# Performance work log

Hardware: AMD Instinct MI355X
Metric: run time of the kernel (lower is better)

The kernel has to match this reference:

```python
import jax, jax.numpy as jnp
import numpy as np

DIM = 768
NUM_HEADS = 12
HEAD_DIM = DIM // NUM_HEADS
ALL_HEAD_DIM = HEAD_DIM * NUM_HEADS
SCALE = HEAD_DIM ** -0.5


def setup_inputs() -> dict:
    key = jax.random.key(0)
    k1, k2, k3, k4 = jax.random.split(key, 4)
    B, N = 8, 1024
    x = jax.random.normal(k1, (B, N, DIM), dtype=jnp.float32)
    # qkv_bias=False -> no qkv bias; proj has bias (nn.Linear default)
    w_qkv = jax.random.normal(k2, (DIM, 3 * ALL_HEAD_DIM), dtype=jnp.float32) * (DIM ** -0.5)
    w_proj = jax.random.normal(k3, (ALL_HEAD_DIM, DIM), dtype=jnp.float32) * (ALL_HEAD_DIM ** -0.5)
    b_proj = jax.random.normal(k4, (DIM,), dtype=jnp.float32) * 0.02
    return {"x": x, "w_qkv": w_qkv, "w_proj": w_proj, "b_proj": b_proj}


def reference(x, w_qkv, w_proj, b_proj):
    B, N, C = x.shape
    qkv = (x @ w_qkv).reshape(B, N, 3, NUM_HEADS, HEAD_DIM)
    qkv = jnp.transpose(qkv, (2, 0, 3, 1, 4))  # [3, B, H, N, D]
    q, k, v = qkv[0], qkv[1], qkv[2]
    attn = jax.nn.softmax(jnp.einsum('bhnd,bhmd->bhnm', q * SCALE, k), axis=-1)
    out = jnp.einsum('bhnm,bhmd->bhnd', attn, v)  # [B, H, N, D]
    out = jnp.transpose(out, (0, 2, 1, 3)).reshape(B, N, ALL_HEAD_DIM)
    return out @ w_proj + b_proj
```

## Files before the change

kernel.cpp:

```cpp
#include <hip/hip_runtime.h>

#define NH 12
#define HD 64
#define SEQ 1024
#define BATCH 8
#define DIM 768
#define QKVN 2304
#define ROWS 8192

typedef __bf16 bf16x8 __attribute__((ext_vector_type(8)));
typedef float f32x4 __attribute__((ext_vector_type(4)));
typedef unsigned short u16x8 __attribute__((ext_vector_type(8)));
typedef unsigned short u16x4 __attribute__((ext_vector_type(4)));
typedef short s16x4 __attribute__((ext_vector_type(4)));

__device__ __forceinline__ unsigned short f2bf(float f) {
  union { float f; unsigned int u; } c; c.f = f;
  unsigned int u = c.u;
  u += 0x7fffu + ((u >> 16) & 1u);
  return (unsigned short)(u >> 16);
}

__device__ __forceinline__ void gload_lds16(const unsigned short* g, unsigned short* l) {
  __builtin_amdgcn_global_load_lds(
      (const __attribute__((address_space(1))) void*)g,
      (__attribute__((address_space(3))) void*)l, 16, 0, 0);
}

__global__ void cvt_bf16(const float* __restrict__ src, unsigned short* __restrict__ dst, int n4) {
  int i = blockIdx.x * 256 + threadIdx.x;
  if (i >= n4) return;
  float4 v = ((const float4*)src)[i];
  u16x4 o;
  o.x = f2bf(v.x); o.y = f2bf(v.y); o.z = f2bf(v.z); o.w = f2bf(v.w);
  ((u16x4*)dst)[i] = o;
}

__global__ void transpose_bf16(const float* __restrict__ src, unsigned short* __restrict__ dst,
                               int R, int C) {
  __shared__ float tile[32][33];
  int tx = threadIdx.x & 31, ty = threadIdx.x >> 5;
  int c0 = blockIdx.x * 32, r0 = blockIdx.y * 32;
#pragma unroll
  for (int i = 0; i < 4; ++i)
    tile[ty + i * 8][tx] = src[(size_t)(r0 + ty + i * 8) * C + c0 + tx];
  __syncthreads();
#pragma unroll
  for (int i = 0; i < 4; ++i)
    dst[(size_t)(c0 + ty + i * 8) * R + r0 + tx] = f2bf(tile[tx][ty + i * 8]);
}

template <bool BF16_OUT, bool SCALE_Q>
__global__ __launch_bounds__(256, 3) void gemm128(
    const unsigned short* __restrict__ A, const unsigned short* __restrict__ BT,
    void* __restrict__ Cout, const float* __restrict__ bias, int M, int N, int K) {
  __shared__ unsigned short As[128 * 32];
  __shared__ unsigned short Bs[128 * 32];
  const int tid = threadIdx.x;
  const int wave = tid >> 6, lane = tid & 63, quad = lane >> 4, l16 = lane & 15;
  const int wm = wave >> 1, wn = wave & 1;
  const int bm = blockIdx.y * 128, bn = blockIdx.x * 128;

  f32x4 zero4 = {0.f, 0.f, 0.f, 0.f};
  f32x4 acc[4][4];
#pragma unroll
  for (int i = 0; i < 4; ++i)
#pragma unroll
    for (int j = 0; j < 4; ++j) acc[i][j] = zero4;

  const int nkt = K >> 5;
  for (int kt = 0; kt < nkt; ++kt) {
    __syncthreads();
    const int k0 = kt * 32;
#pragma unroll
    for (int i = 0; i < 2; ++i) {
      int c0 = wave * 64 + 256 * i;
      int c = c0 + lane;
      int r = c >> 2, kc = c & 3;
      gload_lds16(A + (size_t)(bm + r) * K + k0 + kc * 8, &As[c0 * 8]);
    }
#pragma unroll
    for (int i = 0; i < 2; ++i) {
      int c0 = wave * 64 + 256 * i;
      int c = c0 + lane;
      int r = c >> 2, kc = c & 3;
      gload_lds16(BT + (size_t)(bn + r) * K + k0 + kc * 8, &Bs[c0 * 8]);
    }
    __syncthreads();
    bf16x8 af[4], bf[4];
#pragma unroll
    for (int mt = 0; mt < 4; ++mt)
      af[mt] = *(const bf16x8*)&As[(wm * 64 + mt * 16 + l16) * 32 + quad * 8];
#pragma unroll
    for (int nt = 0; nt < 4; ++nt)
      bf[nt] = *(const bf16x8*)&Bs[(wn * 64 + nt * 16 + l16) * 32 + quad * 8];
#pragma unroll
    for (int mt = 0; mt < 4; ++mt)
#pragma unroll
      for (int nt = 0; nt < 4; ++nt)
        acc[mt][nt] = __builtin_amdgcn_mfma_f32_16x16x32_bf16(af[mt], bf[nt], acc[mt][nt], 0, 0, 0);
  }
#pragma unroll
  for (int mt = 0; mt < 4; ++mt)
#pragma unroll
    for (int nt = 0; nt < 4; ++nt) {
      int col = bn + wn * 64 + nt * 16 + l16;
      float bv = BF16_OUT ? 0.f : bias[col];
      float scl = (SCALE_Q && col < DIM) ? 0.125f : 1.0f;
#pragma unroll
      for (int r = 0; r < 4; ++r) {
        int row = bm + wm * 64 + mt * 16 + quad * 4 + r;
        float v = acc[mt][nt][r];
        if (BF16_OUT)
          ((unsigned short*)Cout)[(size_t)row * N + col] = f2bf(v * scl);
        else
          ((float*)Cout)[(size_t)row * N + col] = v + bv;
      }
    }
}

#define VS 76
__global__ __launch_bounds__(512, 6) void attn_kernel(
    const unsigned short* __restrict__ qkv, unsigned short* __restrict__ out) {
  __shared__ unsigned short Ks[2][64 * 64];
  __shared__ unsigned short Vts[2][64 * VS];

  const int tid = threadIdx.x;
  const int wave = tid >> 6, lane = tid & 63, quad = lane >> 4, l16 = lane & 15;
  const int x = blockIdx.x;
  const int qt = (x >> 3) & 7;
  const int bh = (x & 7) + 8 * (x >> 6);
  const int b = bh / NH, h = bh % NH;
  const int qcol = h * HD, kcol = DIM + h * HD, vcol = 2 * DIM + h * HD;
  const int rowQ0 = b * SEQ + qt * 128;
  const int rowKV0 = b * SEQ;

  const int kk_s = tid >> 8, rem_s = tid & 255, n_s = rem_s >> 2, kc_s = rem_s & 3;
  const unsigned short* kgp = qkv + (size_t)(rowKV0 + n_s) * QKVN + kcol + kk_s * 32 + kc_s * 8;
  unsigned short* klp = &Ks[0][0] + (tid & ~63) * 8;
  const int vn = tid & 63, vd0 = (tid >> 6) * 8;
  const unsigned short* vgp = qkv + (size_t)(rowKV0 + vn) * QKVN + vcol + vd0;

  bf16x8 qf[2];
  {
    const unsigned short* qp = qkv + (size_t)(rowQ0 + wave * 16 + l16) * QKVN + qcol + quad * 8;
    qf[0] = *(const bf16x8*)qp;
    qf[1] = *(const bf16x8*)(qp + 32);
  }

  u16x8 vreg = *(const u16x8*)vgp;
  gload_lds16(kgp, klp);
  {
    unsigned short* vb = &Vts[0][0];
#pragma unroll
    for (int e = 0; e < 8; ++e)
      vb[(vd0 + e) * VS + vn] = vreg[e];
  }

  f32x4 zero4 = {0.f, 0.f, 0.f, 0.f};
  f32x4 o[4];
#pragma unroll
  for (int dt = 0; dt < 4; ++dt) o[dt] = zero4;
  float lsum = 0.f;

  for (int jt = 0; jt < 16; ++jt) {
    u16x8 vnext;
    if (jt < 15) vnext = *(const u16x8*)(vgp + (size_t)(jt + 1) * 64 * QKVN);
    __syncthreads();
    if (jt < 15)
      gload_lds16(kgp + (size_t)(jt + 1) * 64 * QKVN, klp + ((jt + 1) & 1) * 4096);

    const unsigned short* Kb = &Ks[jt & 1][0];
    const unsigned short* Vb = &Vts[jt & 1][0];

    f32x4 s[4];
#pragma unroll
    for (int nt = 0; nt < 4; ++nt) s[nt] = zero4;
#pragma unroll
    for (int kk = 0; kk < 2; ++kk)
#pragma unroll
      for (int nt = 0; nt < 4; ++nt) {
        bf16x8 kf = *(const bf16x8*)&Kb[kk * 2048 + (nt * 16 + l16) * 32 + quad * 8];
        s[nt] = __builtin_amdgcn_mfma_f32_16x16x32_bf16(kf, qf[kk], s[nt], 0, 0, 0);
      }

    s16x4 pf[4];
#pragma unroll
    for (int nt = 0; nt < 4; ++nt)
#pragma unroll
      for (int r = 0; r < 4; ++r) {
        float p = __expf(s[nt][r]);
        lsum += p;
        pf[nt][r] = (short)f2bf(p);
      }

#pragma unroll
    for (int nt = 0; nt < 4; ++nt)
#pragma unroll
      for (int dt = 0; dt < 4; ++dt) {
        s16x4 vv = *(const s16x4*)&Vb[(dt * 16 + l16) * VS + nt * 16 + quad * 4];
        o[dt] = __builtin_amdgcn_mfma_f32_16x16x16bf16_1k(pf[nt], vv, o[dt], 0, 0, 0);
      }

    if (jt < 15) {
      unsigned short* vb = &Vts[(jt + 1) & 1][0];
#pragma unroll
      for (int e = 0; e < 8; ++e)
        vb[(vd0 + e) * VS + vn] = vnext[e];
    }
  }

  float l = lsum;
  l += __shfl_xor(l, 16);
  l += __shfl_xor(l, 32);
#pragma unroll
  for (int r = 0; r < 4; ++r) {
    float inv = 1.f / __shfl(l, quad * 4 + r);
    int row = rowQ0 + wave * 16 + quad * 4 + r;
#pragma unroll
    for (int dt = 0; dt < 4; ++dt)
      out[(size_t)row * DIM + h * HD + dt * 16 + l16] = f2bf(o[dt][r] * inv);
  }
}

extern "C" void kernel_launch(void* const* d_in, const int* in_sizes, int n_in,
                              void* d_out, int out_size, void* d_ws, size_t ws_size,
                              hipStream_t stream) {
  const float* x = (const float*)d_in[0];
  const float* w_qkv = (const float*)d_in[1];
  const float* w_proj = (const float*)d_in[2];
  const float* b_proj = (const float*)d_in[3];
  float* outp = (float*)d_out;

  unsigned short* xb = (unsigned short*)d_ws;
  unsigned short* wqkvT = xb + (size_t)ROWS * DIM;
  unsigned short* wprojT = wqkvT + (size_t)QKVN * DIM;
  unsigned short* qkvb = wprojT + (size_t)DIM * DIM;
  unsigned short* attnb = xb;

  cvt_bf16<<<(ROWS * DIM / 4 + 255) / 256, 256, 0, stream>>>(x, xb, ROWS * DIM / 4);
  transpose_bf16<<<dim3(QKVN / 32, DIM / 32), 256, 0, stream>>>(w_qkv, wqkvT, DIM, QKVN);
  transpose_bf16<<<dim3(DIM / 32, DIM / 32), 256, 0, stream>>>(w_proj, wprojT, DIM, DIM);
  gemm128<true, true><<<dim3(QKVN / 128, ROWS / 128), 256, 0, stream>>>(xb, wqkvT, qkvb, nullptr, ROWS, QKVN, DIM);
  attn_kernel<<<dim3(8 * 96), 512, 0, stream>>>(qkvb, attnb);
  gemm128<false, false><<<dim3(DIM / 128, ROWS / 128), 256, 0, stream>>>(attnb, wprojT, outp, b_proj, ROWS, DIM, DIM);
}
```

Before: 199.7 us.

## Double-buffer GEMM LDS tiles, remap blocks per XCD, raise occupancy hint

The bf16 GEMM now keeps two LDS stages for the A and B tiles. It issues the global-to-LDS loads for the next k-tile right after a single barrier per iteration, so loads can overlap MFMA work on the current tile. The 2D grid becomes a 1D grid with a remap that gives each group of 8 row-blocks to one XCD, which is meant to improve L2 reuse of A rows. The launch-bounds occupancy hint rises from 3 to 5 blocks. The cost is double the LDS per block and a reliance on the compiler's waitcnt placement to keep the prefetch both correct and overlapped.

Measured after the change: 211.3 us. 5.8% more time.

```diff
diff --git a/kernel.cpp b/kernel.cpp
--- a/kernel.cpp
+++ b/kernel.cpp
@@ -51,15 +51,34 @@
 }
 
 template <bool BF16_OUT, bool SCALE_Q>
-__global__ __launch_bounds__(256, 3) void gemm128(
+__global__ __launch_bounds__(256, 5) void gemm128(
     const unsigned short* __restrict__ A, const unsigned short* __restrict__ BT,
-    void* __restrict__ Cout, const float* __restrict__ bias, int M, int N, int K) {
-  __shared__ unsigned short As[128 * 32];
-  __shared__ unsigned short Bs[128 * 32];
+    void* __restrict__ Cout, const float* __restrict__ bias,
+    int M, int N, int K, int nbx, int nbyXCD) {
+  __shared__ unsigned short As[2][128 * 32];
+  __shared__ unsigned short Bs[2][128 * 32];
   const int tid = threadIdx.x;
   const int wave = tid >> 6, lane = tid & 63, quad = lane >> 4, l16 = lane & 15;
   const int wm = wave >> 1, wn = wave & 1;
-  const int bm = blockIdx.y * 128, bn = blockIdx.x * 128;
+  const int g = blockIdx.x & 7, bi = blockIdx.x >> 3;
+  const int by = g * nbyXCD + (bi % nbyXCD);
+  const int bx = bi / nbyXCD;
+  const int bm = by * 128, bn = bx * 128;
+
+  const int r0 = tid >> 2, kc0 = (tid & 3) * 8;
+  const unsigned short* Ag = A + (size_t)(bm + r0) * K + kc0;
+  const unsigned short* Bg = BT + (size_t)(bn + r0) * K + kc0;
+  unsigned short* AsB = &As[0][0];
+  unsigned short* BsB = &Bs[0][0];
+  const int wdst = (tid & ~63) * 8;
+
+#define STAGE_G(kt, b) do {                                                   \
+    int koff_ = (kt) * 32;                                                    \
+    gload_lds16(Ag + koff_,                    AsB + (b) * 4096 + wdst);      \
+    gload_lds16(Ag + koff_ + (size_t)64 * K,   AsB + (b) * 4096 + wdst + 2048);\
+    gload_lds16(Bg + koff_,                    BsB + (b) * 4096 + wdst);      \
+    gload_lds16(Bg + koff_ + (size_t)64 * K,   BsB + (b) * 4096 + wdst + 2048);\
+  } while (0)
 
   f32x4 zero4 = {0.f, 0.f, 0.f, 0.f};
   f32x4 acc[4][4];
@@ -69,37 +88,27 @@
     for (int j = 0; j < 4; ++j) acc[i][j] = zero4;
 
   const int nkt = K >> 5;
+  STAGE_G(0, 0);
   for (int kt = 0; kt < nkt; ++kt) {
     __syncthreads();
-    const int k0 = kt * 32;
-#pragma unroll
-    for (int i = 0; i < 2; ++i) {
-      int c0 = wave * 64 + 256 * i;
-      int c = c0 + lane;
-      int r = c >> 2, kc = c & 3;
-      gload_lds16(A + (size_t)(bm + r) * K + k0 + kc * 8, &As[c0 * 8]);
-    }
-#pragma unroll
-    for (int i = 0; i < 2; ++i) {
-      int c0 = wave * 64 + 256 * i;
-      int c = c0 + lane;
-      int r = c >> 2, kc = c & 3;
-      gload_lds16(BT + (size_t)(bn + r) * K + k0 + kc * 8, &Bs[c0 * 8]);
-    }
-    __syncthreads();
+    if (kt + 1 < nkt) STAGE_G(kt + 1, (kt + 1) & 1);
+    const unsigned short* Ab = AsB + (kt & 1) * 4096;
+    const unsigned short* Bb = BsB + (kt & 1) * 4096;
     bf16x8 af[4], bf[4];
 #pragma unroll
     for (int mt = 0; mt < 4; ++mt)
-      af[mt] = *(const bf16x8*)&As[(wm * 64 + mt * 16 + l16) * 32 + quad * 8];
+      af[mt] = *(const bf16x8*)&Ab[(wm * 64 + mt * 16 + l16) * 32 + quad * 8];
 #pragma unroll
     for (int nt = 0; nt < 4; ++nt)
-      bf[nt] = *(const bf16x8*)&Bs[(wn * 64 + nt * 16 + l16) * 32 + quad * 8];
+      bf[nt] = *(const bf16x8*)&Bb[(wn * 64 + nt * 16 + l16) * 32 + quad * 8];
 #pragma unroll
     for (int mt = 0; mt < 4; ++mt)
 #pragma unroll
       for (int nt = 0; nt < 4; ++nt)
         acc[mt][nt] = __builtin_amdgcn_mfma_f32_16x16x32_bf16(af[mt], bf[nt], acc[mt][nt], 0, 0, 0);
   }
+#undef STAGE_G
+
 #pragma unroll
   for (int mt = 0; mt < 4; ++mt)
 #pragma unroll
@@ -241,7 +250,7 @@
   cvt_bf16<<<(ROWS * DIM / 4 + 255) / 256, 256, 0, stream>>>(x, xb, ROWS * DIM / 4);
   transpose_bf16<<<dim3(QKVN / 32, DIM / 32), 256, 0, stream>>>(w_qkv, wqkvT, DIM, QKVN);
   transpose_bf16<<<dim3(DIM / 32, DIM / 32), 256, 0, stream>>>(w_proj, wprojT, DIM, DIM);
-  gemm128<true, true><<<dim3(QKVN / 128, ROWS / 128), 256, 0, stream>>>(xb, wqkvT, qkvb, nullptr, ROWS, QKVN, DIM);
+  gemm128<true, true><<<dim3(1152), 256, 0, stream>>>(xb, wqkvT, qkvb, nullptr, ROWS, QKVN, DIM, 18, 8);
   attn_kernel<<<dim3(8 * 96), 512, 0, stream>>>(qkvb, attnb);
-  gemm128<false, false><<<dim3(DIM / 128, ROWS / 128), 256, 0, stream>>>(attnb, wprojT, outp, b_proj, ROWS, DIM, DIM);
-}
+  gemm128<false, false><<<dim3(384), 256, 0, stream>>>(attnb, wprojT, outp, b_proj, ROWS, DIM, DIM, 6, 8);
+}
```
